# Kernel tuning notes

Measured on AMD Instinct MI355X. Metric: run time of the kernel, lower is better.

The kernel has to match this reference:

```python
import jax, jax.numpy as jnp
import numpy as np

INPUT, HIDDEN, OUTPUT = 512, 1024, 512

def setup_inputs() -> dict:
    key = jax.random.key(0)
    ks = jax.random.split(key, 7)
    B, T = 64, 1024
    s_ih = 1.0 / np.sqrt(HIDDEN)
    x = jax.random.normal(ks[0], (B, T, INPUT), dtype=jnp.float32)
    W_ih = jax.random.uniform(ks[1], (HIDDEN, INPUT), minval=-s_ih, maxval=s_ih, dtype=jnp.float32)
    W_hh = jax.random.uniform(ks[2], (HIDDEN, HIDDEN), minval=-s_ih, maxval=s_ih, dtype=jnp.float32)
    b_ih = jax.random.uniform(ks[3], (HIDDEN,), minval=-s_ih, maxval=s_ih, dtype=jnp.float32)
    b_hh = jax.random.uniform(ks[4], (HIDDEN,), minval=-s_ih, maxval=s_ih, dtype=jnp.float32)
    s_o = 1.0 / np.sqrt(HIDDEN)
    W_out = jax.random.uniform(ks[5], (OUTPUT, HIDDEN), minval=-s_o, maxval=s_o, dtype=jnp.float32)
    b_out = jax.random.uniform(ks[6], (OUTPUT,), minval=-s_o, maxval=s_o, dtype=jnp.float32)
    return {"x": x, "W_ih": W_ih, "W_hh": W_hh, "b_ih": b_ih, "b_hh": b_hh,
            "W_out": W_out, "b_out": b_out}

def reference(x, W_ih, W_hh, b_ih, b_hh, W_out, b_out):
    B = x.shape[0]
    # Precompute input projection for all timesteps: [B, T, H]
    xp = jnp.einsum('bti,hi->bth', x, W_ih) + b_ih + b_hh
    h0 = jnp.zeros((B, W_hh.shape[0]), dtype=x.dtype)

    def step(h, xp_t):
        h_new = jnp.tanh(xp_t + h @ W_hh.T)
        return h_new, h_new

    _, hs = jax.lax.scan(step, h0, jnp.swapaxes(xp, 0, 1))  # hs: [T, B, H]
    hs = jnp.swapaxes(hs, 0, 1)  # [B, T, H]
    # Per-step output head, batched over all timesteps
    return jnp.einsum('bth,oh->bto', hs, W_out) + b_out
```

## Files before the change

### kernel.cpp

```cpp
#include <hip/hip_runtime.h>

typedef __attribute__((ext_vector_type(8))) short s16x8;
typedef __attribute__((ext_vector_type(4))) float fx4;

static __device__ __forceinline__ unsigned short f2bf(float f){
  unsigned u = __float_as_uint(f);
  return (unsigned short)((u + 0x7fffu + ((u>>16)&1u)) >> 16);
}
static __device__ __forceinline__ float bf2f(unsigned short s){
  return __uint_as_float(((unsigned)s)<<16);
}

__global__ void k_cvt_wout(const float* __restrict__ w, unsigned short* __restrict__ o){
  int g = blockIdx.x*256 + threadIdx.x;
  int idx = g*4;
  float4 f = *(const float4*)(w + idx);
  unsigned u0 = (unsigned)f2bf(f.x) | ((unsigned)f2bf(f.y)<<16);
  unsigned u1 = (unsigned)f2bf(f.z) | ((unsigned)f2bf(f.w)<<16);
  *(uint2*)(o + idx) = make_uint2(u0, u1);
}

__global__ __launch_bounds__(256) void k_gemm_xp(
    const float* __restrict__ X, const float* __restrict__ Wih,
    const float* __restrict__ bih, const float* __restrict__ bhh,
    unsigned short* __restrict__ XP){
  __shared__ unsigned short As[128][40];
  __shared__ unsigned short Bs[128][40];
  const int bm = blockIdx.x, bn = blockIdx.y;
  const int tid = threadIdx.x, w = tid>>6, l = tid&63;
  const int wm = w>>1, wn = w&1;
  const int m0 = bm*128, n0 = bn*128;
  fx4 acc[4][4] = {};
  for (int kb = 0; kb < 512; kb += 32){
    #pragma unroll
    for (int q=0;q<4;q++){
      int f = tid + q*256;
      int row = f>>3, c4 = (f&7)*4;
      float4 v = *(const float4*)(X + (m0+row)*512 + kb + c4);
      unsigned u0 = (unsigned)f2bf(v.x) | ((unsigned)f2bf(v.y)<<16);
      unsigned u1 = (unsigned)f2bf(v.z) | ((unsigned)f2bf(v.w)<<16);
      *(uint2*)&As[row][c4] = make_uint2(u0,u1);
    }
    #pragma unroll
    for (int q=0;q<4;q++){
      int f = tid + q*256;
      int row = f>>3, c4 = (f&7)*4;
      float4 v = *(const float4*)(Wih + (n0+row)*512 + kb + c4);
      unsigned u0 = (unsigned)f2bf(v.x) | ((unsigned)f2bf(v.y)<<16);
      unsigned u1 = (unsigned)f2bf(v.z) | ((unsigned)f2bf(v.w)<<16);
      *(uint2*)&Bs[row][c4] = make_uint2(u0,u1);
    }
    __syncthreads();
    const int kbase = (l>>4)*8;
    s16x8 a[4], b[4];
    #pragma unroll
    for (int mt=0;mt<4;mt++) a[mt] = *(const s16x8*)&As[wm*64 + mt*16 + (l&15)][kbase];
    #pragma unroll
    for (int nt=0;nt<4;nt++) b[nt] = *(const s16x8*)&Bs[wn*64 + nt*16 + (l&15)][kbase];
    #pragma unroll
    for (int mt=0;mt<4;mt++)
      #pragma unroll
      for (int nt=0;nt<4;nt++)
        acc[mt][nt] = __builtin_amdgcn_mfma_f32_16x16x32_bf16(a[mt], b[nt], acc[mt][nt], 0,0,0);
    __syncthreads();
  }
  #pragma unroll
  for (int nt=0;nt<4;nt++){
    int n = n0 + wn*64 + nt*16 + (l&15);
    float bias = bih[n] + bhh[n];
    #pragma unroll
    for (int mt=0;mt<4;mt++){
      #pragma unroll
      for (int r=0;r<4;r++){
        int grow = m0 + wm*64 + mt*16 + (l>>4)*4 + r;
        int bb = grow >> 10, t = grow & 1023;
        XP[(t*64 + bb)*1024 + n] = f2bf(acc[mt][nt][r] + bias);
      }
    }
  }
}

__global__ __launch_bounds__(256) void k_rnn(
    const float* __restrict__ Whh, const unsigned short* __restrict__ XP,
    unsigned short* __restrict__ HS, unsigned* __restrict__ ctrl){
  __shared__ unsigned short hlds[8][1032];
  const int wg = blockIdx.x;
  const int gi = wg & 7;
  const int gj = wg >> 3;
  const int bi = gi*8, cj = gj*64;
  const int tid = threadIdx.x, w = tid>>6, l = tid&63;
  const int kbase = (l>>4)*8;
  unsigned* flags = ctrl + 256;
  unsigned* fc    = ctrl + 4096 + gi*32;

  unsigned xcd;
  asm volatile("s_getreg_b32 %0, hwreg(HW_REG_XCC_ID)" : "=s"(xcd));
  xcd = (xcd & 0xffu) | 0x100u;
  if (tid==0){
    __hip_atomic_store(&ctrl[16+wg], xcd, __ATOMIC_RELAXED, __HIP_MEMORY_SCOPE_AGENT);
    __hip_atomic_fetch_add(&ctrl[0], 1u, __ATOMIC_RELEASE, __HIP_MEMORY_SCOPE_AGENT);
    while (__hip_atomic_load(&ctrl[0], __ATOMIC_RELAXED, __HIP_MEMORY_SCOPE_AGENT) < 128u){}
  }
  __syncthreads();
  bool ok = true;
  if (l < 16){
    unsigned peer = __hip_atomic_load(&ctrl[16 + l*8 + gi], __ATOMIC_RELAXED, __HIP_MEMORY_SCOPE_AGENT);
    ok = (peer == xcd);
  }
  const bool local = __all(ok);

  const int col = cj + w*16 + (l&15);
  s16x8 wf[32];
  #pragma unroll
  for (int kk=0; kk<32; kk++){
    const float* p = Whh + col*1024 + kk*32 + kbase;
    float4 v0 = *(const float4*)p;
    float4 v1 = *(const float4*)(p+4);
    s16x8 s;
    s[0]=(short)f2bf(v0.x); s[1]=(short)f2bf(v0.y); s[2]=(short)f2bf(v0.z); s[3]=(short)f2bf(v0.w);
    s[4]=(short)f2bf(v1.x); s[5]=(short)f2bf(v1.y); s[6]=(short)f2bf(v1.z); s[7]=(short)f2bf(v1.w);
    wf[kk]=s;
  }

  const int ecol = cj + w*16 + (l&15);
  if (l < 32){
    #pragma unroll
    for (int r=0;r<4;r++){
      int row = (l>>4)*4 + r;
      float xv = bf2f(XP[(bi+row)*1024 + ecol]);
      unsigned short hv = f2bf(tanhf(xv));
      if (local) HS[((bi+row)*1024 + 0)*1024 + ecol] = hv;
      else __hip_atomic_store(&HS[((bi+row)*1024+0)*1024+ecol], hv,
                              __ATOMIC_RELAXED, __HIP_MEMORY_SCOPE_AGENT);
    }
  }
  asm volatile("s_waitcnt vmcnt(0)" ::: "memory");
  __syncthreads();
  if (tid==0){
    if (local) __hip_atomic_store(&flags[(gi*16+gj)*16], 1u, __ATOMIC_RELAXED, __HIP_MEMORY_SCOPE_AGENT);
    else __hip_atomic_fetch_add(fc, 1u, __ATOMIC_RELEASE, __HIP_MEMORY_SCOPE_AGENT);
  }

  for (int s=1; s<1024; ++s){
    float xv[4];
    if (l < 32){
      #pragma unroll
      for (int r=0;r<4;r++)
        xv[r] = bf2f(XP[(s*64 + bi + (l>>4)*4 + r)*1024 + ecol]);
    }
    if (local){
      if (tid < 16){
        for(;;){
          unsigned v = __hip_atomic_load(&flags[(gi*16+tid)*16], __ATOMIC_RELAXED, __HIP_MEMORY_SCOPE_AGENT);
          if (__all(v >= (unsigned)s)) break;
        }
      }
    } else {
      if (tid==0){
        while (__hip_atomic_load(fc, __ATOMIC_RELAXED, __HIP_MEMORY_SCOPE_AGENT) < 16u*(unsigned)s){}
      }
    }
    __syncthreads();
    {
      int r0 = w*2 + (l>>5);
      int c0 = (l&31)*8;
      const unsigned short* rowp = HS + ((bi + r0)*1024 + (s-1))*1024;
      #pragma unroll
      for (int j=0;j<4;j++)
        *(uint4*)&hlds[r0][c0 + j*256] = *(const uint4*)(rowp + c0 + j*256);
    }
    __syncthreads();
    const int arow = (l&15)&7;
    fx4 ac0 = {0.f,0.f,0.f,0.f}, ac1 = ac0, ac2 = ac0, ac3 = ac0;
    #pragma unroll
    for (int kk=0;kk<32;kk+=4){
      s16x8 a0 = *(const s16x8*)&hlds[arow][(kk+0)*32 + kbase];
      s16x8 a1 = *(const s16x8*)&hlds[arow][(kk+1)*32 + kbase];
      s16x8 a2 = *(const s16x8*)&hlds[arow][(kk+2)*32 + kbase];
      s16x8 a3 = *(const s16x8*)&hlds[arow][(kk+3)*32 + kbase];
      ac0 = __builtin_amdgcn_mfma_f32_16x16x32_bf16(a0, wf[kk+0], ac0, 0,0,0);
      ac1 = __builtin_amdgcn_mfma_f32_16x16x32_bf16(a1, wf[kk+1], ac1, 0,0,0);
      ac2 = __builtin_amdgcn_mfma_f32_16x16x32_bf16(a2, wf[kk+2], ac2, 0,0,0);
      ac3 = __builtin_amdgcn_mfma_f32_16x16x32_bf16(a3, wf[kk+3], ac3, 0,0,0);
    }
    fx4 acc = (ac0+ac1)+(ac2+ac3);
    if (l < 32){
      #pragma unroll
      for (int r=0;r<4;r++){
        int row = (l>>4)*4 + r;
        float h = tanhf(acc[r] + xv[r]);
        unsigned short hv = f2bf(h);
        if (local) HS[((bi+row)*1024 + s)*1024 + ecol] = hv;
        else __hip_atomic_store(&HS[((bi+row)*1024+s)*1024+ecol], hv,
                                __ATOMIC_RELAXED, __HIP_MEMORY_SCOPE_AGENT);
      }
    }
    asm volatile("s_waitcnt vmcnt(0)" ::: "memory");
    __syncthreads();
    if (tid==0){
      if (local) __hip_atomic_store(&flags[(gi*16+gj)*16], (unsigned)(s+1), __ATOMIC_RELAXED, __HIP_MEMORY_SCOPE_AGENT);
      else __hip_atomic_fetch_add(fc, 1u, __ATOMIC_RELEASE, __HIP_MEMORY_SCOPE_AGENT);
    }
  }
}

__global__ __launch_bounds__(512) void k_gemm_out(
    const unsigned short* __restrict__ HS, const unsigned short* __restrict__ WoutB,
    const float* __restrict__ bout, float* __restrict__ OUT){
  __shared__ unsigned short As[128][40];
  __shared__ unsigned short Bs[512][40];
  const int m0 = blockIdx.x*128;
  const int tid = threadIdx.x, w = tid>>6, l = tid&63;
  const int wm = w>>2, wn = w&3;
  fx4 acc[4][8] = {};
  for (int kb = 0; kb < 1024; kb += 32){
    {
      int row = tid>>2, c8 = (tid&3)*8;
      *(uint4*)&As[row][c8] = *(const uint4*)(HS + (m0+row)*1024 + kb + c8);
    }
    #pragma unroll
    for (int q=0;q<4;q++){
      int f = tid + q*512;
      int row = f>>2, c8 = (f&3)*8;
      *(uint4*)&Bs[row][c8] = *(const uint4*)(WoutB + row*1024 + kb + c8);
    }
    __syncthreads();
    const int kbase = (l>>4)*8;
    s16x8 a[4], b[8];
    #pragma unroll
    for (int mt=0;mt<4;mt++) a[mt] = *(const s16x8*)&As[wm*64 + mt*16 + (l&15)][kbase];
    #pragma unroll
    for (int nt=0;nt<8;nt++) b[nt] = *(const s16x8*)&Bs[wn*128 + nt*16 + (l&15)][kbase];
    #pragma unroll
    for (int mt=0;mt<4;mt++)
      #pragma unroll
      for (int nt=0;nt<8;nt++)
        acc[mt][nt] = __builtin_amdgcn_mfma_f32_16x16x32_bf16(a[mt], b[nt], acc[mt][nt], 0,0,0);
    __syncthreads();
  }
  #pragma unroll
  for (int nt=0;nt<8;nt++){
    int n = wn*128 + nt*16 + (l&15);
    float bias = bout[n];
    #pragma unroll
    for (int mt=0;mt<4;mt++){
      #pragma unroll
      for (int r=0;r<4;r++){
        int row = m0 + wm*64 + mt*16 + (l>>4)*4 + r;
        OUT[row*512 + n] = acc[mt][nt][r] + bias;
      }
    }
  }
}

extern "C" void kernel_launch(void* const* d_in, const int* in_sizes, int n_in,
                              void* d_out, int out_size, void* d_ws, size_t ws_size,
                              hipStream_t stream){
  const float* x    = (const float*)d_in[0];
  const float* Wih  = (const float*)d_in[1];
  const float* Whh  = (const float*)d_in[2];
  const float* bih  = (const float*)d_in[3];
  const float* bhh  = (const float*)d_in[4];
  const float* Wout = (const float*)d_in[5];
  const float* bout = (const float*)d_in[6];

  const size_t XP_BYTES = 134217728ull;
  unsigned short* XP    = (unsigned short*)d_ws;
  unsigned short* WoutB = (unsigned short*)((char*)d_ws + XP_BYTES);
  unsigned*       ctrl  = (unsigned*)((char*)d_ws + XP_BYTES + 1048576ull);
  unsigned short* HS    = (unsigned short*)d_out;
  float*          OUT   = (float*)d_out;

  hipMemsetAsync(ctrl, 0, 32768, stream);
  k_cvt_wout<<<512, 256, 0, stream>>>(Wout, WoutB);
  dim3 g1(512, 8);
  k_gemm_xp<<<g1, 256, 0, stream>>>(x, Wih, bih, bhh, XP);
  k_rnn<<<128, 256, 0, stream>>>(Whh, XP, HS, ctrl);
  k_gemm_out<<<512, 512, 0, stream>>>(HS, WoutB, bout, OUT);
}
```

Baseline: 3.049 ms.

## Poll step flags via L2-scoped loads with periodic agent-scope fallback in RNN

Result: slower. 4.848 ms (+59.0%).

```diff
diff --git a/kernel.cpp b/kernel.cpp
--- a/kernel.cpp
+++ b/kernel.cpp
@@ -9,6 +9,13 @@
 }
 static __device__ __forceinline__ float bf2f(unsigned short s){
   return __uint_as_float(((unsigned)s)<<16);
+}
+static __device__ __forceinline__ unsigned ld_flag_sc0(const unsigned* p){
+  unsigned v;
+  asm volatile("global_load_dword %0, %1, off sc0\n\t"
+               "s_waitcnt vmcnt(0)"
+               : "=v"(v) : "v"(p) : "memory");
+  return v;
 }
 
 __global__ void k_cvt_wout(const float* __restrict__ w, unsigned short* __restrict__ o){
@@ -90,8 +97,9 @@
   const int bi = gi*8, cj = gj*64;
   const int tid = threadIdx.x, w = tid>>6, l = tid&63;
   const int kbase = (l>>4)*8;
-  unsigned* flags = ctrl + 256;
-  unsigned* fc    = ctrl + 4096 + gi*32;
+  unsigned* flags  = ctrl + 1024;
+  unsigned* flagsL = ctrl + 12288;
+  unsigned* fc     = ctrl + 8192 + gi*32;
 
   unsigned xcd;
   asm volatile("s_getreg_b32 %0, hwreg(HW_REG_XCC_ID)" : "=s"(xcd));
@@ -137,30 +145,44 @@
   asm volatile("s_waitcnt vmcnt(0)" ::: "memory");
   __syncthreads();
   if (tid==0){
-    if (local) __hip_atomic_store(&flags[(gi*16+gj)*16], 1u, __ATOMIC_RELAXED, __HIP_MEMORY_SCOPE_AGENT);
-    else __hip_atomic_fetch_add(fc, 1u, __ATOMIC_RELEASE, __HIP_MEMORY_SCOPE_AGENT);
+    if (local){
+      __hip_atomic_store(&flags[(gi*16+gj)*32], 1u,
+                         __ATOMIC_RELAXED, __HIP_MEMORY_SCOPE_WORKGROUP);
+      __hip_atomic_store(&flagsL[(gi*16+gj)*32], 1u,
+                         __ATOMIC_RELAXED, __HIP_MEMORY_SCOPE_AGENT);
+    } else {
+      __hip_atomic_fetch_add(fc, 1u, __ATOMIC_RELEASE, __HIP_MEMORY_SCOPE_AGENT);
+    }
   }
 
   for (int s=1; s<1024; ++s){
-    float xv[4];
-    if (l < 32){
-      #pragma unroll
-      for (int r=0;r<4;r++)
-        xv[r] = bf2f(XP[(s*64 + bi + (l>>4)*4 + r)*1024 + ecol]);
-    }
     if (local){
-      if (tid < 16){
-        for(;;){
-          unsigned v = __hip_atomic_load(&flags[(gi*16+tid)*16], __ATOMIC_RELAXED, __HIP_MEMORY_SCOPE_AGENT);
-          if (__all(v >= (unsigned)s)) break;
+      const unsigned* fpL2  = &flags [(gi*16 + (l&15))*32];
+      const unsigned* fpLLC = &flagsL[(gi*16 + (l&15))*32];
+      unsigned it = 0;
+      for(;;){
+        unsigned v = 0xFFFFFFFFu;
+        if (l < 16){
+          v = ld_flag_sc0(fpL2);
+          if (((++it) & 15u) == 0u){
+            unsigned v2 = __hip_atomic_load(fpLLC, __ATOMIC_RELAXED, __HIP_MEMORY_SCOPE_AGENT);
+            v = (v > v2) ? v : v2;
+          }
         }
+        if (__all(v >= (unsigned)s)) break;
       }
     } else {
       if (tid==0){
         while (__hip_atomic_load(fc, __ATOMIC_RELAXED, __HIP_MEMORY_SCOPE_AGENT) < 16u*(unsigned)s){}
       }
-    }
-    __syncthreads();
+      __syncthreads();
+    }
+    float xv[4];
+    if (l < 32){
+      #pragma unroll
+      for (int r=0;r<4;r++)
+        xv[r] = bf2f(XP[(s*64 + bi + (l>>4)*4 + r)*1024 + ecol]);
+    }
     {
       int r0 = w*2 + (l>>5);
       int c0 = (l&31)*8;
@@ -198,8 +220,14 @@
     asm volatile("s_waitcnt vmcnt(0)" ::: "memory");
     __syncthreads();
     if (tid==0){
-      if (local) __hip_atomic_store(&flags[(gi*16+gj)*16], (unsigned)(s+1), __ATOMIC_RELAXED, __HIP_MEMORY_SCOPE_AGENT);
-      else __hip_atomic_fetch_add(fc, 1u, __ATOMIC_RELEASE, __HIP_MEMORY_SCOPE_AGENT);
+      if (local){
+        __hip_atomic_store(&flags[(gi*16+gj)*32], (unsigned)(s+1),
+                           __ATOMIC_RELAXED, __HIP_MEMORY_SCOPE_WORKGROUP);
+        __hip_atomic_store(&flagsL[(gi*16+gj)*32], (unsigned)(s+1),
+                           __ATOMIC_RELAXED, __HIP_MEMORY_SCOPE_AGENT);
+      } else {
+        __hip_atomic_fetch_add(fc, 1u, __ATOMIC_RELEASE, __HIP_MEMORY_SCOPE_AGENT);
+      }
     }
   }
 }
@@ -271,7 +299,7 @@
   unsigned short* HS    = (unsigned short*)d_out;
   float*          OUT   = (float*)d_out;
 
-  hipMemsetAsync(ctrl, 0, 32768, stream);
+  hipMemsetAsync(ctrl, 0, 65536, stream);
   k_cvt_wout<<<512, 256, 0, stream>>>(Wout, WoutB);
   dim3 g1(512, 8);
   k_gemm_xp<<<g1, 256, 0, stream>>>(x, Wih, bih, bhh, XP);
```

## Halve RNN workgroups to 64 and use per-wave flags without block barriers

Applied to the files above, without the earlier changes.

Result: slower. 3.472 ms (+13.9%).

```diff
diff --git a/kernel.cpp b/kernel.cpp
--- a/kernel.cpp
+++ b/kernel.cpp
@@ -9,6 +9,15 @@
 }
 static __device__ __forceinline__ float bf2f(unsigned short s){
   return __uint_as_float(((unsigned)s)<<16);
+}
+static __device__ __forceinline__ void ld2_g128_sc1(const void* p0, const void* p1,
+                                                    uint4* o0, uint4* o1){
+  uint4 a, b;
+  asm volatile("global_load_dwordx4 %0, %2, off sc1\n\t"
+               "global_load_dwordx4 %1, %3, off sc1\n\t"
+               "s_waitcnt vmcnt(0)"
+               : "=&v"(a), "=&v"(b) : "v"(p0), "v"(p1) : "memory");
+  *o0 = a; *o1 = b;
 }
 
 __global__ void k_cvt_wout(const float* __restrict__ w, unsigned short* __restrict__ o){
@@ -80,18 +89,18 @@
   }
 }
 
-__global__ __launch_bounds__(256) void k_rnn(
+__global__ __launch_bounds__(512) void k_rnn(
     const float* __restrict__ Whh, const unsigned short* __restrict__ XP,
     unsigned short* __restrict__ HS, unsigned* __restrict__ ctrl){
   __shared__ unsigned short hlds[8][1032];
   const int wg = blockIdx.x;
   const int gi = wg & 7;
   const int gj = wg >> 3;
-  const int bi = gi*8, cj = gj*64;
+  const int bi = gi*8, cj = gj*128;
   const int tid = threadIdx.x, w = tid>>6, l = tid&63;
   const int kbase = (l>>4)*8;
-  unsigned* flags = ctrl + 256;
-  unsigned* fc    = ctrl + 4096 + gi*32;
+  unsigned* flags = ctrl + 1024;
+  unsigned* fc    = ctrl + 8192 + gi*32;
 
   unsigned xcd;
   asm volatile("s_getreg_b32 %0, hwreg(HW_REG_XCC_ID)" : "=s"(xcd));
@@ -99,12 +108,12 @@
   if (tid==0){
     __hip_atomic_store(&ctrl[16+wg], xcd, __ATOMIC_RELAXED, __HIP_MEMORY_SCOPE_AGENT);
     __hip_atomic_fetch_add(&ctrl[0], 1u, __ATOMIC_RELEASE, __HIP_MEMORY_SCOPE_AGENT);
-    while (__hip_atomic_load(&ctrl[0], __ATOMIC_RELAXED, __HIP_MEMORY_SCOPE_AGENT) < 128u){}
+    while (__hip_atomic_load(&ctrl[0], __ATOMIC_RELAXED, __HIP_MEMORY_SCOPE_AGENT) < 64u){}
   }
   __syncthreads();
   bool ok = true;
-  if (l < 16){
-    unsigned peer = __hip_atomic_load(&ctrl[16 + l*8 + gi], __ATOMIC_RELAXED, __HIP_MEMORY_SCOPE_AGENT);
+  if (l < 8){
+    unsigned peer = __hip_atomic_load(&ctrl[16 + gi + l*8], __ATOMIC_RELAXED, __HIP_MEMORY_SCOPE_AGENT);
     ok = (peer == xcd);
   }
   const bool local = __all(ok);
@@ -123,22 +132,23 @@
   }
 
   const int ecol = cj + w*16 + (l&15);
-  if (l < 32){
-    #pragma unroll
-    for (int r=0;r<4;r++){
-      int row = (l>>4)*4 + r;
-      float xv = bf2f(XP[(bi+row)*1024 + ecol]);
-      unsigned short hv = f2bf(tanhf(xv));
-      if (local) HS[((bi+row)*1024 + 0)*1024 + ecol] = hv;
-      else __hip_atomic_store(&HS[((bi+row)*1024+0)*1024+ecol], hv,
-                              __ATOMIC_RELAXED, __HIP_MEMORY_SCOPE_AGENT);
-    }
+  unsigned* myflag = &flags[gi*256 + gj*32 + w*4];
+
+  {
+    int e = tid*2;
+    int row = e>>7, c = e&127;
+    unsigned short h0 = f2bf(tanhf(bf2f(XP[(bi+row)*1024 + cj + c])));
+    unsigned short h1 = f2bf(tanhf(bf2f(XP[(bi+row)*1024 + cj + c + 1])));
+    unsigned pk = (unsigned)h0 | ((unsigned)h1<<16);
+    __hip_atomic_store((unsigned*)&HS[((bi+row)*1024 + 0)*1024 + cj + c], pk,
+                       __ATOMIC_RELAXED, __HIP_MEMORY_SCOPE_AGENT);
   }
   asm volatile("s_waitcnt vmcnt(0)" ::: "memory");
-  __syncthreads();
-  if (tid==0){
-    if (local) __hip_atomic_store(&flags[(gi*16+gj)*16], 1u, __ATOMIC_RELAXED, __HIP_MEMORY_SCOPE_AGENT);
-    else __hip_atomic_fetch_add(fc, 1u, __ATOMIC_RELEASE, __HIP_MEMORY_SCOPE_AGENT);
+  if (local){
+    if (l==0) __hip_atomic_store(myflag, 1u, __ATOMIC_RELAXED, __HIP_MEMORY_SCOPE_AGENT);
+  } else {
+    __syncthreads();
+    if (tid==0) __hip_atomic_fetch_add(fc, 1u, __ATOMIC_RELEASE, __HIP_MEMORY_SCOPE_AGENT);
   }
 
   for (int s=1; s<1024; ++s){
@@ -149,25 +159,24 @@
         xv[r] = bf2f(XP[(s*64 + bi + (l>>4)*4 + r)*1024 + ecol]);
     }
     if (local){
-      if (tid < 16){
-        for(;;){
-          unsigned v = __hip_atomic_load(&flags[(gi*16+tid)*16], __ATOMIC_RELAXED, __HIP_MEMORY_SCOPE_AGENT);
-          if (__all(v >= (unsigned)s)) break;
-        }
+      const unsigned* fp = &flags[gi*256 + l*4];
+      for(;;){
+        unsigned v = __hip_atomic_load(fp, __ATOMIC_RELAXED, __HIP_MEMORY_SCOPE_AGENT);
+        if (__all(v >= (unsigned)s)) break;
       }
     } else {
       if (tid==0){
-        while (__hip_atomic_load(fc, __ATOMIC_RELAXED, __HIP_MEMORY_SCOPE_AGENT) < 16u*(unsigned)s){}
-      }
-    }
-    __syncthreads();
+        while (__hip_atomic_load(fc, __ATOMIC_RELAXED, __HIP_MEMORY_SCOPE_AGENT) < 8u*(unsigned)s){}
+      }
+      __syncthreads();
+    }
     {
-      int r0 = w*2 + (l>>5);
-      int c0 = (l&31)*8;
-      const unsigned short* rowp = HS + ((bi + r0)*1024 + (s-1))*1024;
-      #pragma unroll
-      for (int j=0;j<4;j++)
-        *(uint4*)&hlds[r0][c0 + j*256] = *(const uint4*)(rowp + c0 + j*256);
+      int row = tid>>6, c8 = (tid&63)*16;
+      const unsigned short* rowp = HS + ((bi+row)*1024 + (s-1))*1024 + c8;
+      uint4 v0, v1;
+      ld2_g128_sc1(rowp, rowp+8, &v0, &v1);
+      *(uint4*)&hlds[row][c8]     = v0;
+      *(uint4*)&hlds[row][c8 + 8] = v1;
     }
     __syncthreads();
     const int arow = (l&15)&7;
@@ -188,18 +197,18 @@
       #pragma unroll
       for (int r=0;r<4;r++){
         int row = (l>>4)*4 + r;
-        float h = tanhf(acc[r] + xv[r]);
-        unsigned short hv = f2bf(h);
-        if (local) HS[((bi+row)*1024 + s)*1024 + ecol] = hv;
-        else __hip_atomic_store(&HS[((bi+row)*1024+s)*1024+ecol], hv,
-                                __ATOMIC_RELAXED, __HIP_MEMORY_SCOPE_AGENT);
+        unsigned short hv = f2bf(tanhf(acc[r] + xv[r]));
+        __hip_atomic_store(&HS[((bi+row)*1024 + s)*1024 + ecol], hv,
+                           __ATOMIC_RELAXED, __HIP_MEMORY_SCOPE_AGENT);
       }
     }
     asm volatile("s_waitcnt vmcnt(0)" ::: "memory");
-    __syncthreads();
-    if (tid==0){
-      if (local) __hip_atomic_store(&flags[(gi*16+gj)*16], (unsigned)(s+1), __ATOMIC_RELAXED, __HIP_MEMORY_SCOPE_AGENT);
-      else __hip_atomic_fetch_add(fc, 1u, __ATOMIC_RELEASE, __HIP_MEMORY_SCOPE_AGENT);
+    if (local){
+      if (l==0) __hip_atomic_store(myflag, (unsigned)(s+1),
+                                   __ATOMIC_RELAXED, __HIP_MEMORY_SCOPE_AGENT);
+    } else {
+      __syncthreads();
+      if (tid==0) __hip_atomic_fetch_add(fc, 1u, __ATOMIC_RELEASE, __HIP_MEMORY_SCOPE_AGENT);
     }
   }
 }
@@ -271,10 +280,10 @@
   unsigned short* HS    = (unsigned short*)d_out;
   float*          OUT   = (float*)d_out;
 
-  hipMemsetAsync(ctrl, 0, 32768, stream);
+  hipMemsetAsync(ctrl, 0, 65536, stream);
   k_cvt_wout<<<512, 256, 0, stream>>>(Wout, WoutB);
   dim3 g1(512, 8);
   k_gemm_xp<<<g1, 256, 0, stream>>>(x, Wih, bih, bhh, XP);
-  k_rnn<<<128, 256, 0, stream>>>(Whh, XP, HS, ctrl);
+  k_rnn<<<64, 512, 0, stream>>>(Whh, XP, HS, ctrl);
   k_gemm_out<<<512, 512, 0, stream>>>(HS, WoutB, bout, OUT);
 }
```
